# Kernel optimization log

Measured on AMD Instinct MI355X. Metric: run time of the kernel, lower is better.

Reference implementation:

```python
import jax, jax.numpy as jnp
import numpy as np

E, H = 512, 256  # embed_dim, hidden_dim
B, SQ, SK = 2, 512, 512


def _linear_params(k, fin, fout):
    lim = 1.0 / np.sqrt(fin)
    kw, kb = jax.random.split(k)
    W = jax.random.uniform(kw, (fin, fout), minval=-lim, maxval=lim, dtype=jnp.float32)
    b = jax.random.uniform(kb, (fout,), minval=-lim, maxval=lim, dtype=jnp.float32)
    return W, b


def setup_inputs() -> dict:
    rng = jax.random.key(0)
    ks = jax.random.split(rng, 12)
    query = jax.random.normal(ks[0], (B, SQ, E), dtype=jnp.float32)
    key = jax.random.normal(ks[1], (B, SK, E), dtype=jnp.float32)
    Wqe, bqe = _linear_params(ks[2], E, H)
    Wke, bke = _linear_params(ks[3], E, H)
    W1, b1 = _linear_params(ks[4], 2 * H, H)  # importance_predictor layer 0
    W2, b2 = _linear_params(ks[5], H, H)      # layer 1
    W3, b3 = _linear_params(ks[6], H, H)      # layer 2
    Wf, bf = _linear_params(ks[7], H, 1)      # final importance logit
    Wv1, bv1 = _linear_params(ks[8], 2 * H, H)  # variance_estimator layer 0
    Wv2, bv2 = _linear_params(ks[9], H, 1)      # variance_estimator final
    return {"query": query, "key": key,
            "Wqe": Wqe, "bqe": bqe, "Wke": Wke, "bke": bke,
            "W1": W1, "b1": b1, "W2": W2, "b2": b2, "W3": W3, "b3": b3,
            "Wf": Wf, "bf": bf, "Wv1": Wv1, "bv1": bv1, "Wv2": Wv2, "bv2": bv2}


def reference(query, key, Wqe, bqe, Wke, bke, W1, b1, W2, b2, W3, b3, Wf, bf, Wv1, bv1, Wv2, bv2):
    # Encoders (dropout is identity at eval)
    qf = jax.nn.relu(jnp.einsum('bqe,eh->bqh', query, Wqe) + bqe)  # [B,Sq,H]
    kf = jax.nn.relu(jnp.einsum('bke,eh->bkh', key, Wke) + bke)    # [B,Sk,H]

    # First Linear(2H,H) on cat([q,k]) == q@W1[:H] + k@W1[H:]; broadcast over pairs
    qp = jnp.einsum('bqh,hd->bqd', qf, W1[:H])
    kp = jnp.einsum('bkh,hd->bkd', kf, W1[H:])
    h = jax.nn.relu(qp[:, :, None, :] + kp[:, None, :, :] + b1)  # [B,Sq,Sk,H]
    h = jax.nn.relu(jnp.einsum('bqkh,hd->bqkd', h, W2) + b2)
    h = jax.nn.relu(jnp.einsum('bqkh,hd->bqkd', h, W3) + b3)
    importance_logits = (jnp.einsum('bqkh,ho->bqko', h, Wf) + bf)[..., 0]  # [B,Sq,Sk]

    # Variance head: Linear(2H,H) split the same way, ReLU, Linear, Softplus
    vq = jnp.einsum('bqh,hd->bqd', qf, Wv1[:H])
    vk = jnp.einsum('bkh,hd->bkd', kf, Wv1[H:])
    v = jax.nn.relu(vq[:, :, None, :] + vk[:, None, :, :] + bv1)  # [B,Sq,Sk,H]
    estimated_variance = jax.nn.softplus((jnp.einsum('bqkh,ho->bqko', v, Wv2) + bv2)[..., 0])
    return importance_logits, estimated_variance
```

## Files before the change

kernel.cpp:

```cpp
#include <hip/hip_runtime.h>
#include <hip/hip_bf16.h>
#include <cstdint>
#include <cstddef>
#include <cstring>

#define HDIM 256
#define EDIM 512
#define NB   2
#define NSQ  512
#define NSK  512

typedef _Float16 f16x8 __attribute__((ext_vector_type(8)));
typedef _Float16 h2    __attribute__((ext_vector_type(2)));
typedef __fp16   fp16v2 __attribute__((ext_vector_type(2)));
typedef float    f32x4 __attribute__((ext_vector_type(4)));
typedef unsigned short u16x8 __attribute__((ext_vector_type(8)));

#define OFF_W2F  0u
#define OFF_W3F  65536u
#define OFF_WQEF 131072u
#define OFF_WKEF 262144u
#define OFF_WCQ  393216u
#define OFF_WCK  524288u
#define OFF_WV2H 655360u
#define F16_WS_END_BYTES 1312768u

union U8 { f16x8 v; h2 h[4]; };

__device__ __forceinline__ ushort2 f2h2(float x, float y) {
  fp16v2 r = __builtin_amdgcn_cvt_pkrtz(x, y);
  ushort2 u;
  __builtin_memcpy(&u, &r, 4);
  return u;
}
__device__ __forceinline__ float relu_(float x) { return x > 0.f ? x : 0.f; }
__device__ __forceinline__ float softplus_(float x) {
  return fmaxf(x, 0.f) + log1pf(expf(-fabsf(x)));
}

__global__ __launch_bounds__(64) void shuffle_weights(
    const float* __restrict__ Wqe, const float* __restrict__ Wke,
    const float* __restrict__ W1,  const float* __restrict__ Wv1,
    const float* __restrict__ W2,  const float* __restrict__ W3,
    const float* __restrict__ Wv2,
    unsigned short* __restrict__ wsb)
{
  const int bx = blockIdx.x;
  const int lane = threadIdx.x;
  if (bx == 1280) {
    float a = Wv2[lane * 4 + 0], b = Wv2[lane * 4 + 1];
    float c = Wv2[lane * 4 + 2], d = Wv2[lane * 4 + 3];
    ushort2 lo = f2h2(a, b), hi = f2h2(c, d);
    ushort4 o; o.x = lo.x; o.y = lo.y; o.z = hi.x; o.w = hi.y;
    *(ushort4*)&wsb[OFF_WV2H + lane * 4] = o;
    return;
  }
  const float* src; unsigned short* dst; int S; int idx;
  if      (bx <  128) { src = W2;          dst = wsb + OFF_W2F;           S = 8;  idx = bx;        }
  else if (bx <  256) { src = W3;          dst = wsb + OFF_W3F;           S = 8;  idx = bx - 128;  }
  else if (bx <  512) { src = Wqe;         dst = wsb + OFF_WQEF;          S = 16; idx = bx - 256;  }
  else if (bx <  768) { src = Wke;         dst = wsb + OFF_WKEF;          S = 16; idx = bx - 512;  }
  else if (bx <  896) { src = W1;          dst = wsb + OFF_WCQ;           S = 8;  idx = bx - 768;  }
  else if (bx < 1024) { src = Wv1;         dst = wsb + OFF_WCQ + 65536u;  S = 8;  idx = bx - 896;  }
  else if (bx < 1152) { src = W1 + 65536;  dst = wsb + OFF_WCK;           S = 8;  idx = bx - 1024; }
  else                { src = Wv1 + 65536; dst = wsb + OFF_WCK + 65536u;  S = 8;  idx = bx - 1152; }
  const int t = idx / S, s = idx % S;
  const int n  = t * 16 + (lane & 15);
  const int k0 = s * 32 + ((lane >> 4) << 3);
  unsigned short* o = dst + ((size_t)(t * S + s) * 64 + lane) * 8;
  #pragma unroll
  for (int j = 0; j < 8; j += 2) {
    ushort2 pp = f2h2(src[(size_t)(k0 + j) * 256 + n], src[(size_t)(k0 + j + 1) * 256 + n]);
    *(ushort2*)&o[j] = pp;
  }
}

__global__ __launch_bounds__(256) void encoder_kernel(
    const float* __restrict__ query, const float* __restrict__ key,
    const float* __restrict__ bqe,   const float* __restrict__ bke,
    const float* __restrict__ b1,    const float* __restrict__ bv1,
    const unsigned short* __restrict__ WqeF, const unsigned short* __restrict__ WkeF,
    const unsigned short* __restrict__ WcqF, const unsigned short* __restrict__ WckF,
    _Float16* __restrict__ Pq, _Float16* __restrict__ Pk)
{
  __shared__ unsigned short sX[32 * 520];
  __shared__ unsigned short sF[32 * 264];
  __shared__ float sBe[256];
  __shared__ float sBc[512];

  const int bx   = blockIdx.x;
  const int side = bx >> 5;
  const int rt   = bx & 31;
  const int t    = threadIdx.x;

  const float* Xsrc = side ? key : query;
  const unsigned short* WeF = side ? WkeF : WqeF;
  const unsigned short* WcF = side ? WckF : WcqF;
  _Float16* P = side ? Pk : Pq;

  {
    const int m = t >> 3, ch = t & 7;
    const int c0 = ch * 64;
    const float* xr = Xsrc + (size_t)(rt * 32 + m) * EDIM;
    #pragma unroll
    for (int cc = 0; cc < 64; cc += 4) {
      const int c = c0 + cc;
      float4 xv = *(const float4*)(xr + c);
      ushort2 lo = f2h2(xv.x, xv.y);
      ushort2 hi = f2h2(xv.z, xv.w);
      ushort4 xb; xb.x = lo.x; xb.y = lo.y; xb.z = hi.x; xb.w = hi.y;
      *(ushort4*)&sX[m * 520 + c] = xb;
    }
    sBe[t]       = side ? bke[t] : bqe[t];
    sBc[t]       = side ? 0.f : b1[t];
    sBc[256 + t] = side ? 0.f : bv1[t];
  }
  __syncthreads();

  const int wave = t >> 6, lane = t & 63;
  const int l15 = lane & 15, q4 = lane >> 4;

  f32x4 acc1[4][2];
  #pragma unroll
  for (int ft = 0; ft < 4; ++ft)
    #pragma unroll
    for (int pt = 0; pt < 2; ++pt)
      acc1[ft][pt] = (f32x4){0.f, 0.f, 0.f, 0.f};

  for (int s = 0; s < 16; ++s) {
    f16x8 af[4], bfr[2];
    #pragma unroll
    for (int ft = 0; ft < 4; ++ft) {
      const int tg = wave * 4 + ft;
      af[ft] = *(const f16x8*)(WeF + ((size_t)(tg * 16 + s) * 64 + lane) * 8);
    }
    #pragma unroll
    for (int pt = 0; pt < 2; ++pt)
      bfr[pt] = *(const f16x8*)&sX[(pt * 16 + l15) * 520 + s * 32 + q4 * 8];
    #pragma unroll
    for (int ft = 0; ft < 4; ++ft)
      #pragma unroll
      for (int pt = 0; pt < 2; ++pt)
        acc1[ft][pt] = __builtin_amdgcn_mfma_f32_16x16x32_f16(af[ft], bfr[pt], acc1[ft][pt], 0, 0, 0);
  }

  #pragma unroll
  for (int ft = 0; ft < 4; ++ft) {
    const int tg = wave * 4 + ft;
    const int n0 = tg * 16 + q4 * 4;
    float4 b4 = *(const float4*)&sBe[n0];
    #pragma unroll
    for (int pt = 0; pt < 2; ++pt) {
      const int mr = pt * 16 + l15;
      f32x4 a = acc1[ft][pt];
      ushort2 lo = f2h2(relu_(a[0] + b4.x), relu_(a[1] + b4.y));
      ushort2 hi = f2h2(relu_(a[2] + b4.z), relu_(a[3] + b4.w));
      ushort4 h; h.x = lo.x; h.y = lo.y; h.z = hi.x; h.w = hi.y;
      *(ushort4*)&sF[mr * 264 + n0] = h;
    }
  }
  __syncthreads();

  f32x4 acc2[8][2];
  #pragma unroll
  for (int ft = 0; ft < 8; ++ft)
    #pragma unroll
    for (int pt = 0; pt < 2; ++pt)
      acc2[ft][pt] = (f32x4){0.f, 0.f, 0.f, 0.f};

  for (int s = 0; s < 8; ++s) {
    f16x8 af[8], bfr[2];
    #pragma unroll
    for (int ft = 0; ft < 8; ++ft) {
      const int tg = wave * 8 + ft;
      af[ft] = *(const f16x8*)(WcF + ((size_t)(tg * 8 + s) * 64 + lane) * 8);
    }
    #pragma unroll
    for (int pt = 0; pt < 2; ++pt)
      bfr[pt] = *(const f16x8*)&sF[(pt * 16 + l15) * 264 + s * 32 + q4 * 8];
    #pragma unroll
    for (int ft = 0; ft < 8; ++ft)
      #pragma unroll
      for (int pt = 0; pt < 2; ++pt)
        acc2[ft][pt] = __builtin_amdgcn_mfma_f32_16x16x32_f16(af[ft], bfr[pt], acc2[ft][pt], 0, 0, 0);
  }

  #pragma unroll
  for (int ft = 0; ft < 8; ++ft) {
    const int tg = wave * 8 + ft;
    const int n0 = tg * 16 + q4 * 4;
    float4 bc = *(const float4*)&sBc[n0];
    #pragma unroll
    for (int pt = 0; pt < 2; ++pt) {
      const int mr = pt * 16 + l15;
      const int row = rt * 32 + mr;
      f32x4 a = acc2[ft][pt];
      ushort2 lo = f2h2(a[0] + bc.x, a[1] + bc.y);
      ushort2 hi = f2h2(a[2] + bc.z, a[3] + bc.w);
      ushort4 o; o.x = lo.x; o.y = lo.y; o.z = hi.x; o.w = hi.y;
      *(ushort4*)((unsigned short*)P + (size_t)row * 512 + n0) = o;
    }
  }
}

__global__ __launch_bounds__(512, 4) void pair_kernel(
    const _Float16* __restrict__ Pq, const _Float16* __restrict__ Pk,
    const unsigned short* __restrict__ W2F, const unsigned short* __restrict__ W3F,
    const float* __restrict__ b2, const float* __restrict__ b3,
    const float* __restrict__ Wf, const float* __restrict__ bfp,
    const unsigned short* __restrict__ Wv2H, const float* __restrict__ bv2p,
    float* __restrict__ out)
{
  __shared__ __align__(16) unsigned char smem[35840];
  unsigned short* sXH = (unsigned short*)smem;
  float* sB2   = (float*)(smem + 32768);
  float* sB3   = (float*)(smem + 33792);
  float* sWf   = (float*)(smem + 34816);
  float* sRed  = (float*)(smem + 32768);

  const int kt = blockIdx.x, qy = blockIdx.y, bz = blockIdx.z;
  const int t = threadIdx.x;
  const _Float16* qpRow = Pq + (size_t)(bz * NSQ + qy) * 512;

  const int wave = t >> 6, lane = t & 63;
  const int l15 = lane & 15, q4 = lane >> 4;
  const int lsw = l15 & 7;

  const unsigned short* a2base = W2F + ((size_t)(wave * 2) * 8 * 64 + lane) * 8;
  const unsigned short* a3base = W3F + ((size_t)(wave * 2) * 8 * 64 + lane) * 8;

  f16x8 afd[2][2];
  afd[0][0] = *(const f16x8*)(a2base);
  afd[0][1] = *(const f16x8*)(a2base + 8 * 64 * 8);

  {
    const int m   = t >> 3;
    const int sub = t & 7;
    const _Float16* kpRow = Pk + (size_t)(bz * NSK + kt * 64 + m) * 512;
    const int msw = (m & 7);
    const f16x8 z8 = {0, 0, 0, 0, 0, 0, 0, 0};
    float vpart = 0.f;
    #pragma unroll
    for (int it = 0; it < 4; ++it) {
      const int c = it * 64 + sub * 8;
      f16x8 q8 = *(const f16x8*)(qpRow + c);
      f16x8 k8 = *(const f16x8*)(kpRow + c);
      f16x8 r  = __builtin_elementwise_max(q8 + k8, z8);
      const int chunk = (c >> 3) ^ msw;
      *(f16x8*)&sXH[m * 256 + chunk * 8] = r;
      f16x8 a8 = *(const f16x8*)(qpRow + 256 + c);
      f16x8 v8 = *(const f16x8*)(kpRow + 256 + c);
      U8 ar; ar.v = __builtin_elementwise_max(a8 + v8, z8);
      U8 w8; w8.v = *(const f16x8*)((const _Float16*)Wv2H + c);
      vpart = __builtin_amdgcn_fdot2(ar.h[0], w8.h[0], vpart, false);
      vpart = __builtin_amdgcn_fdot2(ar.h[1], w8.h[1], vpart, false);
      vpart = __builtin_amdgcn_fdot2(ar.h[2], w8.h[2], vpart, false);
      vpart = __builtin_amdgcn_fdot2(ar.h[3], w8.h[3], vpart, false);
    }
    vpart += __shfl_xor(vpart, 1, 64);
    vpart += __shfl_xor(vpart, 2, 64);
    vpart += __shfl_xor(vpart, 4, 64);
    if (sub == 0) {
      const size_t o = (size_t)(bz * NSQ + qy) * NSK + kt * 64 + m;
      out[(size_t)NB * NSQ * NSK + o] = softplus_(vpart + bv2p[0]);
    }
    if (t < 256) { sB2[t] = b2[t]; sB3[t] = b3[t]; sWf[t] = Wf[t]; }
  }
  __syncthreads();

  f32x4 acc[2][4];
  #pragma unroll
  for (int ft = 0; ft < 2; ++ft)
    #pragma unroll
    for (int pt = 0; pt < 4; ++pt)
      acc[ft][pt] = (f32x4){0.f, 0.f, 0.f, 0.f};

  #pragma unroll
  for (int s = 0; s < 8; ++s) {
    if (s < 7) {
      afd[(s + 1) & 1][0] = *(const f16x8*)(a2base + (size_t)(s + 1) * 512);
      afd[(s + 1) & 1][1] = *(const f16x8*)(a2base + 8 * 64 * 8 + (size_t)(s + 1) * 512);
    }
    f16x8 bfr[4];
    #pragma unroll
    for (int pt = 0; pt < 4; ++pt) {
      const int chunk = ((s << 2) + q4) ^ lsw;
      bfr[pt] = *(const f16x8*)&sXH[(pt * 16 + l15) * 256 + chunk * 8];
    }
    #pragma unroll
    for (int ft = 0; ft < 2; ++ft)
      #pragma unroll
      for (int pt = 0; pt < 4; ++pt)
        acc[ft][pt] = __builtin_amdgcn_mfma_f32_16x16x32_f16(afd[s & 1][ft], bfr[pt], acc[ft][pt], 0, 0, 0);
  }
  __syncthreads();

  afd[0][0] = *(const f16x8*)(a3base);
  afd[0][1] = *(const f16x8*)(a3base + 8 * 64 * 8);

  #pragma unroll
  for (int ft = 0; ft < 2; ++ft) {
    const int tg = wave * 2 + ft;
    const int n0 = tg * 16 + q4 * 4;
    float4 b4 = *(const float4*)&sB2[n0];
    const int chunkS = ((n0 >> 3) ^ lsw);
    #pragma unroll
    for (int pt = 0; pt < 4; ++pt) {
      const int mr = pt * 16 + l15;
      f32x4 a = acc[ft][pt];
      ushort2 lo = f2h2(relu_(a[0] + b4.x), relu_(a[1] + b4.y));
      ushort2 hi = f2h2(relu_(a[2] + b4.z), relu_(a[3] + b4.w));
      ushort4 h; h.x = lo.x; h.y = lo.y; h.z = hi.x; h.w = hi.y;
      *(ushort4*)&sXH[mr * 256 + chunkS * 8 + (n0 & 7)] = h;
    }
  }
  __syncthreads();

  f32x4 acc2[2][4];
  #pragma unroll
  for (int ft = 0; ft < 2; ++ft)
    #pragma unroll
    for (int pt = 0; pt < 4; ++pt)
      acc2[ft][pt] = (f32x4){0.f, 0.f, 0.f, 0.f};

  #pragma unroll
  for (int s = 0; s < 8; ++s) {
    if (s < 7) {
      afd[(s + 1) & 1][0] = *(const f16x8*)(a3base + (size_t)(s + 1) * 512);
      afd[(s + 1) & 1][1] = *(const f16x8*)(a3base + 8 * 64 * 8 + (size_t)(s + 1) * 512);
    }
    f16x8 bfr[4];
    #pragma unroll
    for (int pt = 0; pt < 4; ++pt) {
      const int chunk = ((s << 2) + q4) ^ lsw;
      bfr[pt] = *(const f16x8*)&sXH[(pt * 16 + l15) * 256 + chunk * 8];
    }
    #pragma unroll
    for (int ft = 0; ft < 2; ++ft)
      #pragma unroll
      for (int pt = 0; pt < 4; ++pt)
        acc2[ft][pt] = __builtin_amdgcn_mfma_f32_16x16x32_f16(afd[s & 1][ft], bfr[pt], acc2[ft][pt], 0, 0, 0);
  }

  float p[4] = {0.f, 0.f, 0.f, 0.f};
  #pragma unroll
  for (int ft = 0; ft < 2; ++ft) {
    const int tg = wave * 2 + ft;
    const int n0 = tg * 16 + q4 * 4;
    float4 b4 = *(const float4*)&sB3[n0];
    float4 w4 = *(const float4*)&sWf[n0];
    #pragma unroll
    for (int pt = 0; pt < 4; ++pt) {
      f32x4 a = acc2[ft][pt];
      p[pt] += relu_(a[0] + b4.x) * w4.x + relu_(a[1] + b4.y) * w4.y
             + relu_(a[2] + b4.z) * w4.z + relu_(a[3] + b4.w) * w4.w;
    }
  }
  __syncthreads();
  #pragma unroll
  for (int pt = 0; pt < 4; ++pt) {
    float v = p[pt];
    v += __shfl_xor(v, 16, 64);
    v += __shfl_xor(v, 32, 64);
    if (lane < 16) sRed[wave * 64 + pt * 16 + lane] = v;
  }
  __syncthreads();

  if (t < 64) {
    const size_t o = (size_t)(bz * NSQ + qy) * NSK + kt * 64 + t;
    float lg = bfp[0];
    #pragma unroll
    for (int w = 0; w < 8; ++w) lg += sRed[w * 64 + t];
    out[o] = lg;
  }
}

extern "C" void kernel_launch(void* const* d_in, const int* in_sizes, int n_in,
                              void* d_out, int out_size, void* d_ws, size_t ws_size,
                              hipStream_t stream)
{
  (void)in_sizes; (void)n_in; (void)out_size; (void)ws_size;
  const float* query = (const float*)d_in[0];
  const float* key   = (const float*)d_in[1];
  const float* Wqe   = (const float*)d_in[2];
  const float* bqe   = (const float*)d_in[3];
  const float* Wke   = (const float*)d_in[4];
  const float* bke   = (const float*)d_in[5];
  const float* W1    = (const float*)d_in[6];
  const float* b1    = (const float*)d_in[7];
  const float* W2    = (const float*)d_in[8];
  const float* b2    = (const float*)d_in[9];
  const float* W3    = (const float*)d_in[10];
  const float* b3    = (const float*)d_in[11];
  const float* Wf    = (const float*)d_in[12];
  const float* bf    = (const float*)d_in[13];
  const float* Wv1   = (const float*)d_in[14];
  const float* bv1   = (const float*)d_in[15];
  const float* Wv2   = (const float*)d_in[16];
  const float* bv2   = (const float*)d_in[17];

  unsigned short* wsb = (unsigned short*)d_ws;
  _Float16* Pq = (_Float16*)((char*)d_ws + F16_WS_END_BYTES);
  _Float16* Pk = Pq + (size_t)1024 * 512;
  float* out = (float*)d_out;

  shuffle_weights<<<1281, 64, 0, stream>>>(Wqe, Wke, W1, Wv1, W2, W3, Wv2, wsb);
  encoder_kernel<<<64, 256, 0, stream>>>(query, key, bqe, bke, b1, bv1,
      wsb + OFF_WQEF, wsb + OFF_WKEF, wsb + OFF_WCQ, wsb + OFF_WCK, Pq, Pk);
  pair_kernel<<<dim3(NSK / 64, NSQ, NB), 512, 0, stream>>>(Pq, Pk,
      wsb + OFF_W2F, wsb + OFF_W3F, b2, b3, Wf, bf, wsb + OFF_WV2H, bv2, out);
}
```

Before: 265.3 us.

## Switch pair kernel to 32x32x16 MFMA with 256 threads, retile encoder and shuffle

The pair kernel moves from 16x16x32 MFMAs with 8 waves to 32x32x16 MFMAs with 4 waves, each wave computing a 64x64 output tile. The weight fragments are repacked into the 32-lane layout, and the swizzled LDS layout is replaced by row padding. This aims to cut LDS fragment reads per FLOP and raise MFMA efficiency. The weight-shuffle kernel now stages coalesced float4 loads through LDS, the encoder uses 16-row tiles over twice as many blocks, and the larger accumulators raise register pressure.

```diff
diff --git a/kernel.cpp b/kernel.cpp
--- a/kernel.cpp
+++ b/kernel.cpp
@@ -13,8 +13,8 @@
 typedef _Float16 f16x8 __attribute__((ext_vector_type(8)));
 typedef _Float16 h2    __attribute__((ext_vector_type(2)));
 typedef __fp16   fp16v2 __attribute__((ext_vector_type(2)));
-typedef float    f32x4 __attribute__((ext_vector_type(4)));
-typedef unsigned short u16x8 __attribute__((ext_vector_type(8)));
+typedef float    f32x4  __attribute__((ext_vector_type(4)));
+typedef float    f32x16 __attribute__((ext_vector_type(16)));
 
 #define OFF_W2F  0u
 #define OFF_W3F  65536u
@@ -38,40 +38,76 @@
   return fmaxf(x, 0.f) + log1pf(expf(-fabsf(x)));
 }
 
-__global__ __launch_bounds__(64) void shuffle_weights(
+__global__ __launch_bounds__(256) void shuffle_weights(
     const float* __restrict__ Wqe, const float* __restrict__ Wke,
     const float* __restrict__ W1,  const float* __restrict__ Wv1,
     const float* __restrict__ W2,  const float* __restrict__ W3,
     const float* __restrict__ Wv2,
     unsigned short* __restrict__ wsb)
 {
+  __shared__ float sW[32 * 257];
   const int bx = blockIdx.x;
-  const int lane = threadIdx.x;
-  if (bx == 1280) {
-    float a = Wv2[lane * 4 + 0], b = Wv2[lane * 4 + 1];
-    float c = Wv2[lane * 4 + 2], d = Wv2[lane * 4 + 3];
-    ushort2 lo = f2h2(a, b), hi = f2h2(c, d);
-    ushort4 o; o.x = lo.x; o.y = lo.y; o.z = hi.x; o.w = hi.y;
-    *(ushort4*)&wsb[OFF_WV2H + lane * 4] = o;
+  const int t = threadIdx.x;
+  if (bx == 96) {
+    if (t < 64) {
+      float a = Wv2[t * 4 + 0], b = Wv2[t * 4 + 1];
+      float c = Wv2[t * 4 + 2], d = Wv2[t * 4 + 3];
+      ushort2 lo = f2h2(a, b), hi = f2h2(c, d);
+      ushort4 o; o.x = lo.x; o.y = lo.y; o.z = hi.x; o.w = hi.y;
+      *(ushort4*)&wsb[OFF_WV2H + t * 4] = o;
+    }
     return;
   }
-  const float* src; unsigned short* dst; int S; int idx;
-  if      (bx <  128) { src = W2;          dst = wsb + OFF_W2F;           S = 8;  idx = bx;        }
-  else if (bx <  256) { src = W3;          dst = wsb + OFF_W3F;           S = 8;  idx = bx - 128;  }
-  else if (bx <  512) { src = Wqe;         dst = wsb + OFF_WQEF;          S = 16; idx = bx - 256;  }
-  else if (bx <  768) { src = Wke;         dst = wsb + OFF_WKEF;          S = 16; idx = bx - 512;  }
-  else if (bx <  896) { src = W1;          dst = wsb + OFF_WCQ;           S = 8;  idx = bx - 768;  }
-  else if (bx < 1024) { src = Wv1;         dst = wsb + OFF_WCQ + 65536u;  S = 8;  idx = bx - 896;  }
-  else if (bx < 1152) { src = W1 + 65536;  dst = wsb + OFF_WCK;           S = 8;  idx = bx - 1024; }
-  else                { src = Wv1 + 65536; dst = wsb + OFF_WCK + 65536u;  S = 8;  idx = bx - 1152; }
-  const int t = idx / S, s = idx % S;
-  const int n  = t * 16 + (lane & 15);
-  const int k0 = s * 32 + ((lane >> 4) << 3);
-  unsigned short* o = dst + ((size_t)(t * S + s) * 64 + lane) * 8;
-  #pragma unroll
-  for (int j = 0; j < 8; j += 2) {
-    ushort2 pp = f2h2(src[(size_t)(k0 + j) * 256 + n], src[(size_t)(k0 + j + 1) * 256 + n]);
-    *(ushort2*)&o[j] = pp;
+  const float* src; unsigned short* dst; int s; bool l32; int S;
+  if      (bx < 16) { src = W2;          dst = wsb + OFF_W2F;           s = bx;      l32 = true;  S = 16; }
+  else if (bx < 32) { src = W3;          dst = wsb + OFF_W3F;           s = bx - 16; l32 = true;  S = 16; }
+  else if (bx < 48) { src = Wqe;         dst = wsb + OFF_WQEF;          s = bx - 32; l32 = false; S = 16; }
+  else if (bx < 64) { src = Wke;         dst = wsb + OFF_WKEF;          s = bx - 48; l32 = false; S = 16; }
+  else if (bx < 72) { src = W1;          dst = wsb + OFF_WCQ;           s = bx - 64; l32 = false; S = 8;  }
+  else if (bx < 80) { src = Wv1;         dst = wsb + OFF_WCQ + 65536u;  s = bx - 72; l32 = false; S = 8;  }
+  else if (bx < 88) { src = W1 + 65536;  dst = wsb + OFF_WCK;           s = bx - 80; l32 = false; S = 8;  }
+  else              { src = Wv1 + 65536; dst = wsb + OFF_WCK + 65536u;  s = bx - 88; l32 = false; S = 8;  }
+
+  const int rows  = l32 ? 16 : 32;
+  const int kbase = l32 ? s * 16 : s * 32;
+  for (int it = 0; it < rows / 4; ++it) {
+    const int f4 = it * 256 + t;
+    const int row = f4 >> 6, c4 = (f4 & 63) * 4;
+    float4 v = *(const float4*)(src + (size_t)(kbase + row) * 256 + c4);
+    sW[row * 257 + c4 + 0] = v.x; sW[row * 257 + c4 + 1] = v.y;
+    sW[row * 257 + c4 + 2] = v.z; sW[row * 257 + c4 + 3] = v.w;
+  }
+  __syncthreads();
+
+  const int wave = t >> 6, lane = t & 63;
+  if (l32) {
+    const int n_in = lane & 31, k0 = (lane >> 5) * 8;
+    for (int tt = wave * 2; tt < wave * 2 + 2; ++tt) {
+      const int n = tt * 32 + n_in;
+      float x[8];
+      #pragma unroll
+      for (int j = 0; j < 8; ++j) x[j] = sW[(k0 + j) * 257 + n];
+      ushort2 p0 = f2h2(x[0], x[1]), p1 = f2h2(x[2], x[3]);
+      ushort2 p2 = f2h2(x[4], x[5]), p3 = f2h2(x[6], x[7]);
+      ushort4 lo; lo.x = p0.x; lo.y = p0.y; lo.z = p1.x; lo.w = p1.y;
+      ushort4 hi; hi.x = p2.x; hi.y = p2.y; hi.z = p3.x; hi.w = p3.y;
+      unsigned short* o = dst + ((size_t)(tt * 16 + s) * 64 + lane) * 8;
+      *(ushort4*)&o[0] = lo; *(ushort4*)&o[4] = hi;
+    }
+  } else {
+    const int n_in = lane & 15, k0 = (lane >> 4) * 8;
+    for (int tt = wave * 4; tt < wave * 4 + 4; ++tt) {
+      const int n = tt * 16 + n_in;
+      float x[8];
+      #pragma unroll
+      for (int j = 0; j < 8; ++j) x[j] = sW[(k0 + j) * 257 + n];
+      ushort2 p0 = f2h2(x[0], x[1]), p1 = f2h2(x[2], x[3]);
+      ushort2 p2 = f2h2(x[4], x[5]), p3 = f2h2(x[6], x[7]);
+      ushort4 lo; lo.x = p0.x; lo.y = p0.y; lo.z = p1.x; lo.w = p1.y;
+      ushort4 hi; hi.x = p2.x; hi.y = p2.y; hi.z = p3.x; hi.w = p3.y;
+      unsigned short* o = dst + ((size_t)(tt * S + s) * 64 + lane) * 8;
+      *(ushort4*)&o[0] = lo; *(ushort4*)&o[4] = hi;
+    }
   }
 }
 
@@ -83,14 +119,14 @@
     const unsigned short* __restrict__ WcqF, const unsigned short* __restrict__ WckF,
     _Float16* __restrict__ Pq, _Float16* __restrict__ Pk)
 {
-  __shared__ unsigned short sX[32 * 520];
-  __shared__ unsigned short sF[32 * 264];
+  __shared__ unsigned short sX[16 * 520];
+  __shared__ unsigned short sF[16 * 264];
   __shared__ float sBe[256];
   __shared__ float sBc[512];
 
   const int bx   = blockIdx.x;
-  const int side = bx >> 5;
-  const int rt   = bx & 31;
+  const int side = bx >> 6;
+  const int rt   = bx & 63;
   const int t    = threadIdx.x;
 
   const float* Xsrc = side ? key : query;
@@ -99,17 +135,19 @@
   _Float16* P = side ? Pk : Pq;
 
   {
-    const int m = t >> 3, ch = t & 7;
-    const int c0 = ch * 64;
-    const float* xr = Xsrc + (size_t)(rt * 32 + m) * EDIM;
-    #pragma unroll
-    for (int cc = 0; cc < 64; cc += 4) {
-      const int c = c0 + cc;
-      float4 xv = *(const float4*)(xr + c);
-      ushort2 lo = f2h2(xv.x, xv.y);
-      ushort2 hi = f2h2(xv.z, xv.w);
-      ushort4 xb; xb.x = lo.x; xb.y = lo.y; xb.z = hi.x; xb.w = hi.y;
-      *(ushort4*)&sX[m * 520 + c] = xb;
+    const int m = t >> 4, ch = t & 15;
+    const float* xr = Xsrc + (size_t)(rt * 16 + m) * EDIM;
+    #pragma unroll
+    for (int j = 0; j < 4; ++j) {
+      const int c = ch * 32 + j * 8;
+      float4 v0 = *(const float4*)(xr + c);
+      float4 v1 = *(const float4*)(xr + c + 4);
+      ushort2 p0 = f2h2(v0.x, v0.y), p1 = f2h2(v0.z, v0.w);
+      ushort2 p2 = f2h2(v1.x, v1.y), p3 = f2h2(v1.z, v1.w);
+      ushort4 lo; lo.x = p0.x; lo.y = p0.y; lo.z = p1.x; lo.w = p1.y;
+      ushort4 hi; hi.x = p2.x; hi.y = p2.y; hi.z = p3.x; hi.w = p3.y;
+      *(ushort4*)&sX[m * 520 + c] = lo;
+      *(ushort4*)&sX[m * 520 + c + 4] = hi;
     }
     sBe[t]       = side ? bke[t] : bqe[t];
     sBc[t]       = side ? 0.f : b1[t];
@@ -120,28 +158,21 @@
   const int wave = t >> 6, lane = t & 63;
   const int l15 = lane & 15, q4 = lane >> 4;
 
-  f32x4 acc1[4][2];
-  #pragma unroll
-  for (int ft = 0; ft < 4; ++ft)
-    #pragma unroll
-    for (int pt = 0; pt < 2; ++pt)
-      acc1[ft][pt] = (f32x4){0.f, 0.f, 0.f, 0.f};
+  f32x4 acc1[4];
+  #pragma unroll
+  for (int ft = 0; ft < 4; ++ft) acc1[ft] = (f32x4){0.f, 0.f, 0.f, 0.f};
 
   for (int s = 0; s < 16; ++s) {
-    f16x8 af[4], bfr[2];
+    f16x8 af[4], bfr;
     #pragma unroll
     for (int ft = 0; ft < 4; ++ft) {
       const int tg = wave * 4 + ft;
       af[ft] = *(const f16x8*)(WeF + ((size_t)(tg * 16 + s) * 64 + lane) * 8);
     }
-    #pragma unroll
-    for (int pt = 0; pt < 2; ++pt)
-      bfr[pt] = *(const f16x8*)&sX[(pt * 16 + l15) * 520 + s * 32 + q4 * 8];
+    bfr = *(const f16x8*)&sX[l15 * 520 + s * 32 + q4 * 8];
     #pragma unroll
     for (int ft = 0; ft < 4; ++ft)
-      #pragma unroll
-      for (int pt = 0; pt < 2; ++pt)
-        acc1[ft][pt] = __builtin_amdgcn_mfma_f32_16x16x32_f16(af[ft], bfr[pt], acc1[ft][pt], 0, 0, 0);
+      acc1[ft] = __builtin_amdgcn_mfma_f32_16x16x32_f16(af[ft], bfr, acc1[ft], 0, 0, 0);
   }
 
   #pragma unroll
@@ -149,40 +180,29 @@
     const int tg = wave * 4 + ft;
     const int n0 = tg * 16 + q4 * 4;
     float4 b4 = *(const float4*)&sBe[n0];
-    #pragma unroll
-    for (int pt = 0; pt < 2; ++pt) {
-      const int mr = pt * 16 + l15;
-      f32x4 a = acc1[ft][pt];
-      ushort2 lo = f2h2(relu_(a[0] + b4.x), relu_(a[1] + b4.y));
-      ushort2 hi = f2h2(relu_(a[2] + b4.z), relu_(a[3] + b4.w));
-      ushort4 h; h.x = lo.x; h.y = lo.y; h.z = hi.x; h.w = hi.y;
-      *(ushort4*)&sF[mr * 264 + n0] = h;
-    }
-  }
-  __syncthreads();
-
-  f32x4 acc2[8][2];
-  #pragma unroll
-  for (int ft = 0; ft < 8; ++ft)
-    #pragma unroll
-    for (int pt = 0; pt < 2; ++pt)
-      acc2[ft][pt] = (f32x4){0.f, 0.f, 0.f, 0.f};
+    f32x4 a = acc1[ft];
+    ushort2 lo = f2h2(relu_(a[0] + b4.x), relu_(a[1] + b4.y));
+    ushort2 hi = f2h2(relu_(a[2] + b4.z), relu_(a[3] + b4.w));
+    ushort4 h; h.x = lo.x; h.y = lo.y; h.z = hi.x; h.w = hi.y;
+    *(ushort4*)&sF[l15 * 264 + n0] = h;
+  }
+  __syncthreads();
+
+  f32x4 acc2[8];
+  #pragma unroll
+  for (int ft = 0; ft < 8; ++ft) acc2[ft] = (f32x4){0.f, 0.f, 0.f, 0.f};
 
   for (int s = 0; s < 8; ++s) {
-    f16x8 af[8], bfr[2];
+    f16x8 af[8], bfr;
     #pragma unroll
     for (int ft = 0; ft < 8; ++ft) {
       const int tg = wave * 8 + ft;
       af[ft] = *(const f16x8*)(WcF + ((size_t)(tg * 8 + s) * 64 + lane) * 8);
     }
-    #pragma unroll
-    for (int pt = 0; pt < 2; ++pt)
-      bfr[pt] = *(const f16x8*)&sF[(pt * 16 + l15) * 264 + s * 32 + q4 * 8];
+    bfr = *(const f16x8*)&sF[l15 * 264 + s * 32 + q4 * 8];
     #pragma unroll
     for (int ft = 0; ft < 8; ++ft)
-      #pragma unroll
-      for (int pt = 0; pt < 2; ++pt)
-        acc2[ft][pt] = __builtin_amdgcn_mfma_f32_16x16x32_f16(af[ft], bfr[pt], acc2[ft][pt], 0, 0, 0);
+      acc2[ft] = __builtin_amdgcn_mfma_f32_16x16x32_f16(af[ft], bfr, acc2[ft], 0, 0, 0);
   }
 
   #pragma unroll
@@ -190,20 +210,16 @@
     const int tg = wave * 8 + ft;
     const int n0 = tg * 16 + q4 * 4;
     float4 bc = *(const float4*)&sBc[n0];
-    #pragma unroll
-    for (int pt = 0; pt < 2; ++pt) {
-      const int mr = pt * 16 + l15;
-      const int row = rt * 32 + mr;
-      f32x4 a = acc2[ft][pt];
-      ushort2 lo = f2h2(a[0] + bc.x, a[1] + bc.y);
-      ushort2 hi = f2h2(a[2] + bc.z, a[3] + bc.w);
-      ushort4 o; o.x = lo.x; o.y = lo.y; o.z = hi.x; o.w = hi.y;
-      *(ushort4*)((unsigned short*)P + (size_t)row * 512 + n0) = o;
-    }
-  }
-}
-
-__global__ __launch_bounds__(512, 4) void pair_kernel(
+    const int row = rt * 16 + l15;
+    f32x4 a = acc2[ft];
+    ushort2 lo = f2h2(a[0] + bc.x, a[1] + bc.y);
+    ushort2 hi = f2h2(a[2] + bc.z, a[3] + bc.w);
+    ushort4 o; o.x = lo.x; o.y = lo.y; o.z = hi.x; o.w = hi.y;
+    *(ushort4*)((unsigned short*)P + (size_t)row * 512 + n0) = o;
+  }
+}
+
+__global__ __launch_bounds__(256, 4) void pair_kernel(
     const _Float16* __restrict__ Pq, const _Float16* __restrict__ Pk,
     const unsigned short* __restrict__ W2F, const unsigned short* __restrict__ W3F,
     const float* __restrict__ b2, const float* __restrict__ b3,
@@ -211,43 +227,42 @@
     const unsigned short* __restrict__ Wv2H, const float* __restrict__ bv2p,
     float* __restrict__ out)
 {
-  __shared__ __align__(16) unsigned char smem[35840];
+  __shared__ __align__(16) unsigned char smem[36864];
   unsigned short* sXH = (unsigned short*)smem;
-  float* sB2   = (float*)(smem + 32768);
-  float* sB3   = (float*)(smem + 33792);
-  float* sWf   = (float*)(smem + 34816);
-  float* sRed  = (float*)(smem + 32768);
+  float* sB2  = (float*)(smem + 33792);
+  float* sB3  = (float*)(smem + 34816);
+  float* sWf  = (float*)(smem + 35840);
+  float* sRed = (float*)(smem + 33792);
 
   const int kt = blockIdx.x, qy = blockIdx.y, bz = blockIdx.z;
   const int t = threadIdx.x;
   const _Float16* qpRow = Pq + (size_t)(bz * NSQ + qy) * 512;
 
   const int wave = t >> 6, lane = t & 63;
-  const int l15 = lane & 15, q4 = lane >> 4;
-  const int lsw = l15 & 7;
-
-  const unsigned short* a2base = W2F + ((size_t)(wave * 2) * 8 * 64 + lane) * 8;
-  const unsigned short* a3base = W3F + ((size_t)(wave * 2) * 8 * 64 + lane) * 8;
+  const int r31 = lane & 31, q = lane >> 5;
+
+  const unsigned short* a2b0 = W2F + ((size_t)((wave * 2 + 0) * 16) * 64 + lane) * 8;
+  const unsigned short* a2b1 = W2F + ((size_t)((wave * 2 + 1) * 16) * 64 + lane) * 8;
+  const unsigned short* a3b0 = W3F + ((size_t)((wave * 2 + 0) * 16) * 64 + lane) * 8;
+  const unsigned short* a3b1 = W3F + ((size_t)((wave * 2 + 1) * 16) * 64 + lane) * 8;
 
   f16x8 afd[2][2];
-  afd[0][0] = *(const f16x8*)(a2base);
-  afd[0][1] = *(const f16x8*)(a2base + 8 * 64 * 8);
+  afd[0][0] = *(const f16x8*)a2b0;
+  afd[0][1] = *(const f16x8*)a2b1;
 
   {
-    const int m   = t >> 3;
-    const int sub = t & 7;
+    const int m   = t >> 2;
+    const int sub = t & 3;
     const _Float16* kpRow = Pk + (size_t)(bz * NSK + kt * 64 + m) * 512;
-    const int msw = (m & 7);
     const f16x8 z8 = {0, 0, 0, 0, 0, 0, 0, 0};
     float vpart = 0.f;
     #pragma unroll
-    for (int it = 0; it < 4; ++it) {
-      const int c = it * 64 + sub * 8;
+    for (int it = 0; it < 8; ++it) {
+      const int c = sub * 64 + it * 8;
       f16x8 q8 = *(const f16x8*)(qpRow + c);
       f16x8 k8 = *(const f16x8*)(kpRow + c);
       f16x8 r  = __builtin_elementwise_max(q8 + k8, z8);
-      const int chunk = (c >> 3) ^ msw;
-      *(f16x8*)&sXH[m * 256 + chunk * 8] = r;
+      *(f16x8*)&sXH[m * 264 + c] = r;
       f16x8 a8 = *(const f16x8*)(qpRow + 256 + c);
       f16x8 v8 = *(const f16x8*)(kpRow + 256 + c);
       U8 ar; ar.v = __builtin_elementwise_max(a8 + v8, z8);
@@ -259,118 +274,118 @@
     }
     vpart += __shfl_xor(vpart, 1, 64);
     vpart += __shfl_xor(vpart, 2, 64);
-    vpart += __shfl_xor(vpart, 4, 64);
     if (sub == 0) {
       const size_t o = (size_t)(bz * NSQ + qy) * NSK + kt * 64 + m;
       out[(size_t)NB * NSQ * NSK + o] = softplus_(vpart + bv2p[0]);
     }
-    if (t < 256) { sB2[t] = b2[t]; sB3[t] = b3[t]; sWf[t] = Wf[t]; }
-  }
-  __syncthreads();
-
-  f32x4 acc[2][4];
-  #pragma unroll
-  for (int ft = 0; ft < 2; ++ft)
-    #pragma unroll
-    for (int pt = 0; pt < 4; ++pt)
-      acc[ft][pt] = (f32x4){0.f, 0.f, 0.f, 0.f};
-
-  #pragma unroll
-  for (int s = 0; s < 8; ++s) {
-    if (s < 7) {
-      afd[(s + 1) & 1][0] = *(const f16x8*)(a2base + (size_t)(s + 1) * 512);
-      afd[(s + 1) & 1][1] = *(const f16x8*)(a2base + 8 * 64 * 8 + (size_t)(s + 1) * 512);
-    }
-    f16x8 bfr[4];
-    #pragma unroll
-    for (int pt = 0; pt < 4; ++pt) {
-      const int chunk = ((s << 2) + q4) ^ lsw;
-      bfr[pt] = *(const f16x8*)&sXH[(pt * 16 + l15) * 256 + chunk * 8];
-    }
-    #pragma unroll
-    for (int ft = 0; ft < 2; ++ft)
-      #pragma unroll
-      for (int pt = 0; pt < 4; ++pt)
-        acc[ft][pt] = __builtin_amdgcn_mfma_f32_16x16x32_f16(afd[s & 1][ft], bfr[pt], acc[ft][pt], 0, 0, 0);
-  }
-  __syncthreads();
-
-  afd[0][0] = *(const f16x8*)(a3base);
-  afd[0][1] = *(const f16x8*)(a3base + 8 * 64 * 8);
-
-  #pragma unroll
-  for (int ft = 0; ft < 2; ++ft) {
-    const int tg = wave * 2 + ft;
-    const int n0 = tg * 16 + q4 * 4;
-    float4 b4 = *(const float4*)&sB2[n0];
-    const int chunkS = ((n0 >> 3) ^ lsw);
-    #pragma unroll
-    for (int pt = 0; pt < 4; ++pt) {
-      const int mr = pt * 16 + l15;
-      f32x4 a = acc[ft][pt];
-      ushort2 lo = f2h2(relu_(a[0] + b4.x), relu_(a[1] + b4.y));
-      ushort2 hi = f2h2(relu_(a[2] + b4.z), relu_(a[3] + b4.w));
-      ushort4 h; h.x = lo.x; h.y = lo.y; h.z = hi.x; h.w = hi.y;
-      *(ushort4*)&sXH[mr * 256 + chunkS * 8 + (n0 & 7)] = h;
-    }
-  }
-  __syncthreads();
-
-  f32x4 acc2[2][4];
-  #pragma unroll
-  for (int ft = 0; ft < 2; ++ft)
-    #pragma unroll
-    for (int pt = 0; pt < 4; ++pt)
-      acc2[ft][pt] = (f32x4){0.f, 0.f, 0.f, 0.f};
-
-  #pragma unroll
-  for (int s = 0; s < 8; ++s) {
-    if (s < 7) {
-      afd[(s + 1) & 1][0] = *(const f16x8*)(a3base + (size_t)(s + 1) * 512);
-      afd[(s + 1) & 1][1] = *(const f16x8*)(a3base + 8 * 64 * 8 + (size_t)(s + 1) * 512);
-    }
-    f16x8 bfr[4];
-    #pragma unroll
-    for (int pt = 0; pt < 4; ++pt) {
-      const int chunk = ((s << 2) + q4) ^ lsw;
-      bfr[pt] = *(const f16x8*)&sXH[(pt * 16 + l15) * 256 + chunk * 8];
-    }
-    #pragma unroll
-    for (int ft = 0; ft < 2; ++ft)
-      #pragma unroll
-      for (int pt = 0; pt < 4; ++pt)
-        acc2[ft][pt] = __builtin_amdgcn_mfma_f32_16x16x32_f16(afd[s & 1][ft], bfr[pt], acc2[ft][pt], 0, 0, 0);
-  }
-
-  float p[4] = {0.f, 0.f, 0.f, 0.f};
-  #pragma unroll
-  for (int ft = 0; ft < 2; ++ft) {
-    const int tg = wave * 2 + ft;
-    const int n0 = tg * 16 + q4 * 4;
-    float4 b4 = *(const float4*)&sB3[n0];
-    float4 w4 = *(const float4*)&sWf[n0];
-    #pragma unroll
-    for (int pt = 0; pt < 4; ++pt) {
-      f32x4 a = acc2[ft][pt];
-      p[pt] += relu_(a[0] + b4.x) * w4.x + relu_(a[1] + b4.y) * w4.y
-             + relu_(a[2] + b4.z) * w4.z + relu_(a[3] + b4.w) * w4.w;
-    }
-  }
-  __syncthreads();
-  #pragma unroll
-  for (int pt = 0; pt < 4; ++pt) {
-    float v = p[pt];
-    v += __shfl_xor(v, 16, 64);
-    v += __shfl_xor(v, 32, 64);
-    if (lane < 16) sRed[wave * 64 + pt * 16 + lane] = v;
+    sB2[t] = b2[t]; sB3[t] = b3[t]; sWf[t] = Wf[t];
+  }
+  __syncthreads();
+
+  f32x16 acc[2][2];
+  #pragma unroll
+  for (int ni = 0; ni < 2; ++ni)
+    #pragma unroll
+    for (int mi = 0; mi < 2; ++mi)
+      #pragma unroll
+      for (int rix = 0; rix < 16; ++rix) acc[ni][mi][rix] = 0.f;
+
+  #pragma unroll
+  for (int s = 0; s < 16; ++s) {
+    if (s < 15) {
+      afd[(s + 1) & 1][0] = *(const f16x8*)(a2b0 + (size_t)(s + 1) * 512);
+      afd[(s + 1) & 1][1] = *(const f16x8*)(a2b1 + (size_t)(s + 1) * 512);
+    }
+    f16x8 bfr[2];
+    #pragma unroll
+    for (int mi = 0; mi < 2; ++mi)
+      bfr[mi] = *(const f16x8*)&sXH[(mi * 32 + r31) * 264 + s * 16 + q * 8];
+    #pragma unroll
+    for (int ni = 0; ni < 2; ++ni)
+      #pragma unroll
+      for (int mi = 0; mi < 2; ++mi)
+        acc[ni][mi] = __builtin_amdgcn_mfma_f32_32x32x16_f16(afd[s & 1][ni], bfr[mi], acc[ni][mi], 0, 0, 0);
+  }
+  __syncthreads();
+
+  afd[0][0] = *(const f16x8*)a3b0;
+  afd[0][1] = *(const f16x8*)a3b1;
+
+  #pragma unroll
+  for (int ni = 0; ni < 2; ++ni) {
+    const int nb = (wave * 2 + ni) * 32;
+    #pragma unroll
+    for (int mi = 0; mi < 2; ++mi) {
+      const int m = mi * 32 + r31;
+      #pragma unroll
+      for (int g = 0; g < 4; ++g) {
+        const int n0 = nb + g * 8 + q * 4;
+        float4 b4 = *(const float4*)&sB2[n0];
+        float x0 = relu_(acc[ni][mi][g * 4 + 0] + b4.x);
+        float x1 = relu_(acc[ni][mi][g * 4 + 1] + b4.y);
+        float x2 = relu_(acc[ni][mi][g * 4 + 2] + b4.z);
+        float x3 = relu_(acc[ni][mi][g * 4 + 3] + b4.w);
+        ushort2 lo = f2h2(x0, x1), hi = f2h2(x2, x3);
+        ushort4 h; h.x = lo.x; h.y = lo.y; h.z = hi.x; h.w = hi.y;
+        *(ushort4*)&sXH[m * 264 + n0] = h;
+      }
+    }
+  }
+  __syncthreads();
+
+  f32x16 acc2[2][2];
+  #pragma unroll
+  for (int ni = 0; ni < 2; ++ni)
+    #pragma unroll
+    for (int mi = 0; mi < 2; ++mi)
+      #pragma unroll
+      for (int rix = 0; rix < 16; ++rix) acc2[ni][mi][rix] = 0.f;
+
+  #pragma unroll
+  for (int s = 0; s < 16; ++s) {
+    if (s < 15) {
+      afd[(s + 1) & 1][0] = *(const f16x8*)(a3b0 + (size_t)(s + 1) * 512);
+      afd[(s + 1) & 1][1] = *(const f16x8*)(a3b1 + (size_t)(s + 1) * 512);
+    }
+    f16x8 bfr[2];
+    #pragma unroll
+    for (int mi = 0; mi < 2; ++mi)
+      bfr[mi] = *(const f16x8*)&sXH[(mi * 32 + r31) * 264 + s * 16 + q * 8];
+    #pragma unroll
+    for (int ni = 0; ni < 2; ++ni)
+      #pragma unroll
+      for (int mi = 0; mi < 2; ++mi)
+        acc2[ni][mi] = __builtin_amdgcn_mfma_f32_32x32x16_f16(afd[s & 1][ni], bfr[mi], acc2[ni][mi], 0, 0, 0);
+  }
+
+  float p[2] = {0.f, 0.f};
+  #pragma unroll
+  for (int ni = 0; ni < 2; ++ni) {
+    const int nb = (wave * 2 + ni) * 32;
+    #pragma unroll
+    for (int g = 0; g < 4; ++g) {
+      const int n0 = nb + g * 8 + q * 4;
+      float4 b4 = *(const float4*)&sB3[n0];
+      float4 w4 = *(const float4*)&sWf[n0];
+      #pragma unroll
+      for (int mi = 0; mi < 2; ++mi) {
+        p[mi] += relu_(acc2[ni][mi][g * 4 + 0] + b4.x) * w4.x
+               + relu_(acc2[ni][mi][g * 4 + 1] + b4.y) * w4.y
+               + relu_(acc2[ni][mi][g * 4 + 2] + b4.z) * w4.z
+               + relu_(acc2[ni][mi][g * 4 + 3] + b4.w) * w4.w;
+      }
+    }
+  }
+  #pragma unroll
+  for (int mi = 0; mi < 2; ++mi) {
+    p[mi] += __shfl_xor(p[mi], 32, 64);
+    if (lane < 32) sRed[wave * 64 + mi * 32 + r31] = p[mi];
   }
   __syncthreads();
 
   if (t < 64) {
     const size_t o = (size_t)(bz * NSQ + qy) * NSK + kt * 64 + t;
-    float lg = bfp[0];
-    #pragma unroll
-    for (int w = 0; w < 8; ++w) lg += sRed[w * 64 + t];
+    float lg = bfp[0] + sRed[t] + sRed[64 + t] + sRed[128 + t] + sRed[192 + t];
     out[o] = lg;
   }
 }
@@ -404,9 +419,9 @@
   _Float16* Pk = Pq + (size_t)1024 * 512;
   float* out = (float*)d_out;
 
-  shuffle_weights<<<1281, 64, 0, stream>>>(Wqe, Wke, W1, Wv1, W2, W3, Wv2, wsb);
-  encoder_kernel<<<64, 256, 0, stream>>>(query, key, bqe, bke, b1, bv1,
+  shuffle_weights<<<97, 256, 0, stream>>>(Wqe, Wke, W1, Wv1, W2, W3, Wv2, wsb);
+  encoder_kernel<<<128, 256, 0, stream>>>(query, key, bqe, bke, b1, bv1,
       wsb + OFF_WQEF, wsb + OFF_WKEF, wsb + OFF_WCQ, wsb + OFF_WCK, Pq, Pk);
-  pair_kernel<<<dim3(NSK / 64, NSQ, NB), 512, 0, stream>>>(Pq, Pk,
+  pair_kernel<<<dim3(NSK / 64, NSQ, NB), 256, 0, stream>>>(Pq, Pk,
       wsb + OFF_W2F, wsb + OFF_W3F, b2, b3, Wf, bf, wsb + OFF_WV2H, bv2, out);
 }
```

New measurement: 316.7 us. +19.4%, slower.
